# Performance work log

Measured on AMD Instinct MI355X. Metric: run time of the kernel, lower is better.

## Reference

```python
import jax, jax.numpy as jnp
import numpy as np
import math

B, N, DIM = 8, 8192, 256
DIM_ATTN, HEAD, RANK = 256, 4, 64
HEAD_DIM = DIM_ATTN // HEAD


def setup_inputs() -> dict:
    key = jax.random.key(0)
    ks = jax.random.split(key, 8)
    x = jax.random.normal(ks[0], (B, N, DIM), dtype=jnp.float32)
    z = jax.random.normal(ks[1], (B, N, DIM), dtype=jnp.float32)
    # nn.Linear(dim, dim_attn): weight (out,in) -> use (in,out) for x @ W
    Wq = jax.random.normal(ks[2], (DIM, DIM_ATTN), dtype=jnp.float32) / np.sqrt(DIM)
    bq = jnp.zeros((DIM_ATTN,), dtype=jnp.float32)
    K = jax.random.normal(ks[3], (RANK, HEAD, HEAD_DIM), dtype=jnp.float32)
    Wv = jax.random.normal(ks[4], (DIM, DIM), dtype=jnp.float32) / np.sqrt(DIM)
    bv = jnp.zeros((DIM,), dtype=jnp.float32)
    alpha = jnp.full((HEAD, 1), math.log(9.0), dtype=jnp.float32)
    beta = jnp.full((HEAD, 1), math.log(0.01), dtype=jnp.float32)
    return {"x": x, "z": z, "Wq": Wq, "bq": bq, "K": K, "Wv": Wv, "bv": bv,
            "alpha": alpha, "beta": beta}


def reference(x, z, Wq, bq, K, Wv, bv, alpha, beta):
    b, n, f = x.shape
    # q: (b, n, head, head_dim)
    q = (z @ Wq + bq).reshape(b, n, HEAD, HEAD_DIM)
    # attn scores over latent rank: (b, n, h, r)
    attn = jnp.einsum('bnhd,rhd->bnhr', q, K) / np.sqrt(HEAD_DIM).astype(np.float32)
    # value projection: (b, n, h, d)
    xv = (x @ Wv + bv).reshape(b, n, HEAD, HEAD_DIM)
    # pool over n with softmax over r: (b, r, h, d)
    pooled = jnp.einsum('bnhr,bnhd->brhd', jax.nn.softmax(attn, axis=-1), xv)
    # redistribute with softmax over n: (b, n, h, d)
    v = jnp.einsum('bnhr,brhd->bnhd', jax.nn.softmax(attn, axis=1), pooled)
    # sigmoid-gated combine; alpha/beta are (head, 1) broadcasting over (h, d)
    out = jax.nn.sigmoid(alpha) * xv + jax.nn.sigmoid(beta) * v
    return out.reshape(b, n, f)
```

## Files before the change

### kernel.cpp

```cpp
#include <hip/hip_runtime.h>
#include <hip/hip_bf16.h>

typedef __hip_bfloat16 bf16;
typedef __attribute__((ext_vector_type(8))) __bf16 bf16x8;
typedef __attribute__((ext_vector_type(4))) float f32x4;

#define BB 8
#define NN 8192
#define DIM 256
#define HEAD 4
#define HD 64
#define RANK 64
#define BN (BB*NN)

__device__ __forceinline__ float b2f(bf16 v){ return __bfloat162float(v); }
__device__ __forceinline__ bf16 f2b(float v){ return __float2bfloat16(v); }
__device__ __forceinline__ unsigned short f2bu(float f){
    bf16 h = __float2bfloat16(f);
    return *(unsigned short*)&h;
}
__device__ __forceinline__ float u2f(unsigned short u){
    unsigned int x = ((unsigned int)u) << 16; return __uint_as_float(x);
}
__device__ __forceinline__ __bf16 f2bb(float f){
    bf16 h = __float2bfloat16(f);
    return *reinterpret_cast<__bf16*>(&h);
}
__device__ __forceinline__ int swz(int k, int outer){
    return (((k >> 3) ^ (outer & 7)) << 3) | (k & 7);
}

__global__ void __launch_bounds__(256) kW(
    const float* __restrict__ Wq, const float* __restrict__ bq,
    const float* __restrict__ Km, const float* __restrict__ Wv,
    unsigned short* __restrict__ WattnT, unsigned short* __restrict__ WvT,
    float* __restrict__ battn, float* __restrict__ pooledZ)
{
    const int c = blockIdx.x;
    const int h = c >> 6, r = c & 63;
    const int t = threadIdx.x;

    {
        int idx = (blockIdx.x*256 + t)*2;
        *(float2*)&pooledZ[idx] = (float2){0.f, 0.f};
    }

    __shared__ float Ks[64];
    if(t < 64) Ks[t] = Km[((size_t)r*HEAD + h)*64 + t];
    __syncthreads();

    const float* wqrow = Wq + (size_t)t*DIM + h*64;
    float a = 0.f;
    #pragma unroll
    for(int d = 0; d < 64; d++) a = fmaf(wqrow[d], Ks[d], a);
    WattnT[(size_t)c*DIM + t] = f2bu(0.125f * a);
    WvT[(size_t)c*DIM + t]    = f2bu(Wv[(size_t)t*DIM + c]);
    if(t == 0){
        float bb = 0.f;
        for(int d = 0; d < 64; d++) bb += bq[h*64+d]*Ks[d];
        battn[c] = 0.125f * bb;
    }
}

__global__ void __launch_bounds__(256) kG(
    const float* __restrict__ x, const float* __restrict__ z,
    const unsigned short* __restrict__ WvT, const unsigned short* __restrict__ WattnT,
    const float* __restrict__ bv, const float* __restrict__ battn,
    float* __restrict__ outF, unsigned short* __restrict__ outB,
    float* __restrict__ Pm, float* __restrict__ Ps)
{
    __shared__ __attribute__((aligned(16))) __bf16 As8[8][64][40];

    const int role = blockIdx.x & 1;
    const int tile = blockIdx.x >> 1;

    const float* A            = role ? z : x;
    const unsigned short* WT  = role ? WattnT : WvT;
    const float* bias         = role ? battn : bv;

    const int t    = threadIdx.x;
    const int lane = t & 63;
    const int w    = t >> 6;
    const int q    = lane >> 4;
    const int l15  = lane & 15;
    const int brow = tile * 64;
    const int arow = t >> 2, aseg = t & 3;

    const float* aSrc = A + (size_t)(brow + arow)*DIM + aseg*8;
    const unsigned short* bBase = WT + (size_t)(w*64 + l15)*DIM + q*8;

    bf16x8 b0[4], b1[4];
    #pragma unroll
    for(int tn = 0; tn < 4; tn++)
        b0[tn] = *(const bf16x8*)(bBase + (size_t)tn*16*DIM);
    #pragma unroll
    for(int tn = 0; tn < 4; tn++)
        b1[tn] = *(const bf16x8*)(bBase + (size_t)tn*16*DIM + 32);

    #pragma unroll
    for(int s = 0; s < 8; s++){
        float4 v0 = *(const float4*)(aSrc + s*32);
        float4 v1 = *(const float4*)(aSrc + s*32 + 4);
        __attribute__((aligned(16))) __bf16 tmp[8] = {
            f2bb(v0.x), f2bb(v0.y), f2bb(v0.z), f2bb(v0.w),
            f2bb(v1.x), f2bb(v1.y), f2bb(v1.z), f2bb(v1.w)};
        *(bf16x8*)&As8[s][arow][aseg*8] = *(bf16x8*)tmp;
    }

    f32x4 acc[4][4];
    #pragma unroll
    for(int tm = 0; tm < 4; tm++)
        #pragma unroll
        for(int tn = 0; tn < 4; tn++) acc[tm][tn] = (f32x4){0.f,0.f,0.f,0.f};

    __syncthreads();

    #pragma unroll
    for(int step = 0; step < 8; step++){
        bf16x8 b2[4];
        if(step < 6){
            #pragma unroll
            for(int tn = 0; tn < 4; tn++)
                b2[tn] = *(const bf16x8*)(bBase + (size_t)tn*16*DIM + (step+2)*32);
        }

        bf16x8 af[4];
        #pragma unroll
        for(int tm = 0; tm < 4; tm++)
            af[tm] = *(const bf16x8*)&As8[step][tm*16 + l15][q*8];

        #pragma unroll
        for(int tm = 0; tm < 4; tm++)
            #pragma unroll
            for(int tn = 0; tn < 4; tn++)
                acc[tm][tn] = __builtin_amdgcn_mfma_f32_16x16x32_bf16(
                    af[tm], b0[tn], acc[tm][tn], 0, 0, 0);

        #pragma unroll
        for(int tn = 0; tn < 4; tn++){ b0[tn] = b1[tn]; b1[tn] = b2[tn]; }
    }

    if(role){
        const int b  = brow >> 13;
        const int nb = brow & 8191;
        const size_t blk = tile;
        #pragma unroll
        for(int tn = 0; tn < 4; tn++){
            int col = w*64 + tn*16 + l15;
            int hh = col >> 6, rr = col & 63;
            float bcol = bias[col];
            float rv[16];
            float m16 = -1e30f;
            #pragma unroll
            for(int tm = 0; tm < 4; tm++){
                #pragma unroll
                for(int reg = 0; reg < 4; reg++){
                    float v = acc[tm][tn][reg] + bcol;
                    unsigned short ub = f2bu(v);
                    int n = nb + tm*16 + q*4 + reg;
                    outB[(((size_t)(b*HEAD + hh))*NN + n)*64 + rr] = ub;
                    float vr = u2f(ub);
                    rv[tm*4+reg] = vr;
                    m16 = fmaxf(m16, vr);
                }
            }
            float s16 = 0.f;
            #pragma unroll
            for(int i = 0; i < 16; i++) s16 += __expf(rv[i] - m16);
            #pragma unroll
            for(int off = 16; off <= 32; off <<= 1){
                float m2 = __shfl_xor(m16, off, 64);
                float s2 = __shfl_xor(s16, off, 64);
                float nm = fmaxf(m16, m2);
                s16 = s16*__expf(m16-nm) + s2*__expf(m2-nm);
                m16 = nm;
            }
            if(q == 0){
                Pm[blk*256 + col] = m16;
                Ps[blk*256 + col] = s16;
            }
        }
    } else {
        #pragma unroll
        for(int tn = 0; tn < 4; tn++){
            int col = w*64 + tn*16 + l15;
            float bcol = bias[col];
            #pragma unroll
            for(int tm = 0; tm < 4; tm++){
                #pragma unroll
                for(int reg = 0; reg < 4; reg++){
                    int grow = brow + tm*16 + q*4 + reg;
                    outF[(size_t)grow*256 + col] = acc[tm][tn][reg] + bcol;
                }
            }
        }
    }
}

__global__ void __launch_bounds__(256) kD(const unsigned short* __restrict__ attn,
                                          const float* __restrict__ xv,
                                          float* __restrict__ pooledT,
                                          const float* __restrict__ Pm, const float* __restrict__ Ps,
                                          float* __restrict__ Mst, float* __restrict__ Sst)
{
    __shared__ unsigned short s1T[64*256];
    __shared__ unsigned short xvT[64*256];

    const int t = threadIdx.x, lane = t & 63, w = t >> 6;
    const int bh = blockIdx.x, chunk = blockIdx.y;
    const int b = bh >> 2, h = bh & 3;
    const int n0 = chunk * 256;
    const int row = t;

    if(chunk == 0 && (bh & 3) == 0){
        const int bb = bh >> 2, col = t;
        float m = -1e30f;
        for(int c = 0; c < 128; c++)
            m = fmaxf(m, Pm[(size_t)(bb*128 + c)*256 + col]);
        float s = 0.f;
        for(int c = 0; c < 128; c++){
            size_t i = (size_t)(bb*128 + c)*256 + col;
            s += Ps[i] * __expf(Pm[i] - m);
        }
        Mst[bb*256 + col] = m;
        Sst[bb*256 + col] = s;
    }

    {
        const uint4* ap = (const uint4*)(attn + ((size_t)bh*NN + n0 + row)*64);
        uint4 ar[8];
        #pragma unroll
        for(int c = 0; c < 8; c++) ar[c] = ap[c];
        float vals[64];
        #pragma unroll
        for(int c = 0; c < 8; c++){
            unsigned int uu[4] = {ar[c].x, ar[c].y, ar[c].z, ar[c].w};
            #pragma unroll
            for(int p = 0; p < 4; p++){
                vals[c*8 + p*2 + 0] = __uint_as_float(uu[p] << 16);
                vals[c*8 + p*2 + 1] = __uint_as_float(uu[p] & 0xffff0000u);
            }
        }
        float mx = -1e30f;
        #pragma unroll
        for(int r = 0; r < 64; r++) mx = fmaxf(mx, vals[r]);
        float s = 0.f;
        #pragma unroll
        for(int r = 0; r < 64; r++){
            float e = __expf(vals[r] - mx);
            s += e;
            s1T[r*256 + swz(row, r)] = f2bu(e);
        }
        float rs = 1.f / s;
        const float4* xp = (const float4*)(xv + ((size_t)(b*NN + n0 + row))*256 + h*64);
        #pragma unroll
        for(int c = 0; c < 16; c++){
            float4 f = xp[c];
            int d0 = c*4;
            xvT[(d0+0)*256 + swz(row, d0+0)] = f2bu(f.x * rs);
            xvT[(d0+1)*256 + swz(row, d0+1)] = f2bu(f.y * rs);
            xvT[(d0+2)*256 + swz(row, d0+2)] = f2bu(f.z * rs);
            xvT[(d0+3)*256 + swz(row, d0+3)] = f2bu(f.w * rs);
        }
    }
    __syncthreads();

    const int q = lane >> 4, l15 = lane & 15;
    const int dm = w*16 + l15;
    f32x4 acc[4];
    #pragma unroll
    for(int tn = 0; tn < 4; tn++) acc[tn] = (f32x4){0.f,0.f,0.f,0.f};

    #pragma unroll
    for(int slab = 0; slab < 8; slab++){
        int c = slab*4 + q;
        bf16x8 a = *(const bf16x8*)&xvT[dm*256 + ((c ^ (dm & 7))<<3)];
        #pragma unroll
        for(int tn = 0; tn < 4; tn++){
            int rn = tn*16 + l15;
            bf16x8 bb = *(const bf16x8*)&s1T[rn*256 + ((c ^ (rn & 7))<<3)];
            acc[tn] = __builtin_amdgcn_mfma_f32_16x16x32_bf16(a, bb, acc[tn], 0, 0, 0);
        }
    }
    #pragma unroll
    for(int tn = 0; tn < 4; tn++){
        #pragma unroll
        for(int reg = 0; reg < 4; reg++){
            int d = w*16 + q*4 + reg;
            int r = tn*16 + l15;
            atomicAdd(&pooledT[((size_t)bh*64 + d)*64 + r], acc[tn][reg]);
        }
    }
}

__global__ void __launch_bounds__(256) kE(const unsigned short* __restrict__ attn,
                                          const float* __restrict__ xvin,
                                          const float* __restrict__ pooledT,
                                          const float* __restrict__ Mst, const float* __restrict__ Sst,
                                          const float* __restrict__ alpha, const float* __restrict__ beta,
                                          float* __restrict__ out)
{
    __shared__ unsigned short s2t[256*64];
    __shared__ unsigned short plT[64*64];
    __shared__ float Ms[64], Sinv[64];

    const int t = threadIdx.x, lane = t & 63, w = t >> 6;
    const int bh = blockIdx.x, chunk = blockIdx.y;
    const int b = bh >> 2, h = bh & 3;
    const int n0 = chunk * 256;
    const int row = t;

    if(t < 64){
        Ms[t]   = Mst[b*256 + h*64 + t];
        Sinv[t] = 1.f / Sst[b*256 + h*64 + t];
    }
    {
        int d = t >> 2, seg = t & 3;
        const float4* pp = (const float4*)(pooledT + ((size_t)bh*64 + d)*64 + seg*16);
        float4 p0 = pp[0], p1 = pp[1], p2 = pp[2], p3 = pp[3];
        __attribute__((aligned(16))) unsigned short tmp[16] = {
            f2bu(p0.x),f2bu(p0.y),f2bu(p0.z),f2bu(p0.w),
            f2bu(p1.x),f2bu(p1.y),f2bu(p1.z),f2bu(p1.w),
            f2bu(p2.x),f2bu(p2.y),f2bu(p2.z),f2bu(p2.w),
            f2bu(p3.x),f2bu(p3.y),f2bu(p3.z),f2bu(p3.w)};
        int c0 = seg*2;
        *(uint4*)&plT[d*64 + (((c0+0) ^ (d&7))<<3)] = *(uint4*)&tmp[0];
        *(uint4*)&plT[d*64 + (((c0+1) ^ (d&7))<<3)] = *(uint4*)&tmp[8];
    }
    __syncthreads();

    {
        const uint4* ap = (const uint4*)(attn + ((size_t)bh*NN + n0 + row)*64);
        #pragma unroll
        for(int c = 0; c < 8; c++){
            uint4 u = ap[c];
            unsigned int uu[4] = {u.x, u.y, u.z, u.w};
            unsigned int ov[4];
            #pragma unroll
            for(int p = 0; p < 4; p++){
                int r = c*8 + p*2;
                float v0 = __uint_as_float(uu[p] << 16);
                float v1 = __uint_as_float(uu[p] & 0xffff0000u);
                float e0 = __expf(v0 - Ms[r])   * Sinv[r];
                float e1 = __expf(v1 - Ms[r+1]) * Sinv[r+1];
                ov[p] = (unsigned int)f2bu(e0) | ((unsigned int)f2bu(e1) << 16);
            }
            uint4 w4; w4.x = ov[0]; w4.y = ov[1]; w4.z = ov[2]; w4.w = ov[3];
            *(uint4*)&s2t[row*64 + ((c ^ (row&7))<<3)] = w4;
        }
    }
    __syncthreads();

    const int q = lane >> 4, l15 = lane & 15;
    f32x4 acc[4][4];
    #pragma unroll
    for(int tm = 0; tm < 4; tm++)
        #pragma unroll
        for(int tn = 0; tn < 4; tn++) acc[tm][tn] = (f32x4){0.f,0.f,0.f,0.f};

    #pragma unroll
    for(int s = 0; s < 2; s++){
        int c = s*4 + q;
        bf16x8 bfr[4], af[4];
        #pragma unroll
        for(int tn = 0; tn < 4; tn++){
            int dn = tn*16 + l15;
            bfr[tn] = *(const bf16x8*)&plT[dn*64 + ((c ^ (dn&7))<<3)];
        }
        #pragma unroll
        for(int tm = 0; tm < 4; tm++){
            int ra = w*64 + tm*16 + l15;
            af[tm] = *(const bf16x8*)&s2t[ra*64 + ((c ^ (ra&7))<<3)];
        }
        #pragma unroll
        for(int tm = 0; tm < 4; tm++)
            #pragma unroll
            for(int tn = 0; tn < 4; tn++)
                acc[tm][tn] = __builtin_amdgcn_mfma_f32_16x16x32_bf16(
                    af[tm], bfr[tn], acc[tm][tn], 0, 0, 0);
    }

    const float sa = 1.f / (1.f + __expf(-alpha[h]));
    const float sb = 1.f / (1.f + __expf(-beta[h]));
    #pragma unroll
    for(int tm = 0; tm < 4; tm++){
        #pragma unroll
        for(int reg = 0; reg < 4; reg++){
            int rowo = w*64 + tm*16 + q*4 + reg;
            size_t gbase = ((size_t)(b*NN + n0 + rowo))*256 + h*64;
            #pragma unroll
            for(int tn = 0; tn < 4; tn++){
                int d = tn*16 + l15;
                out[gbase + d] = sa*xvin[gbase + d] + sb*acc[tm][tn][reg];
            }
        }
    }
}

extern "C" void kernel_launch(void* const* d_in, const int* in_sizes, int n_in,
                              void* d_out, int out_size, void* d_ws, size_t ws_size,
                              hipStream_t stream)
{
    (void)in_sizes; (void)n_in; (void)out_size; (void)ws_size;
    const float* x     = (const float*)d_in[0];
    const float* z     = (const float*)d_in[1];
    const float* Wq    = (const float*)d_in[2];
    const float* bq    = (const float*)d_in[3];
    const float* Km    = (const float*)d_in[4];
    const float* Wv    = (const float*)d_in[5];
    const float* bv    = (const float*)d_in[6];
    const float* alpha = (const float*)d_in[7];
    const float* beta  = (const float*)d_in[8];
    float* out = (float*)d_out;

    float* xv = out;

    char* ws = (char*)d_ws;
    unsigned short* attn  = (unsigned short*)(ws + 0);
    float* pooledT = (float*)(ws + 33554432);
    float* Mst     = (float*)(ws + 34078720);
    float* Sst     = (float*)(ws + 34086912);
    float* Pm      = (float*)(ws + 34095104);
    float* Ps      = (float*)(ws + 35143680);
    unsigned short* WattnT = (unsigned short*)(ws + 36192256);
    unsigned short* WvT    = (unsigned short*)(ws + 36323328);
    float* battn   = (float*)(ws + 36454400);

    kW<<<dim3(256), 256, 0, stream>>>(Wq, bq, Km, Wv, WattnT, WvT, battn, pooledT);
    kG<<<dim3(2*BN/64), 256, 0, stream>>>(x, z, WvT, WattnT, bv, battn, xv, attn, Pm, Ps);
    kD<<<dim3(32, 32), 256, 0, stream>>>(attn, xv, pooledT, Pm, Ps, Mst, Sst);
    kE<<<dim3(32, 32), 256, 0, stream>>>(attn, xv, pooledT, Mst, Sst, alpha, beta, out);
}
```

Measured before the change: 289.3 us.

## Process two row chunks per block in kD/kE with register prefetch of attn

kD and kE now handle two consecutive 256-row chunks per workgroup, halving the grid's y dimension. The attn rows for the second chunk are loaded into registers before the barrier, overlapping their global latency with the first chunk's MFMA work and output. In kD the xv loads are issued earlier into registers. This trades fewer, longer blocks and extra register pressure for hidden load latency and less per-block setup (e.g. the pooled tile conversion in kE).

New measurement: 310.7 us. 7.4% more time.

```diff
diff --git a/kernel.cpp b/kernel.cpp
--- a/kernel.cpp
+++ b/kernel.cpp
@@ -207,12 +207,12 @@
     __shared__ unsigned short xvT[64*256];
 
     const int t = threadIdx.x, lane = t & 63, w = t >> 6;
-    const int bh = blockIdx.x, chunk = blockIdx.y;
+    const int bh = blockIdx.x, cpair = blockIdx.y;
     const int b = bh >> 2, h = bh & 3;
-    const int n0 = chunk * 256;
     const int row = t;
-
-    if(chunk == 0 && (bh & 3) == 0){
+    const int q = lane >> 4, l15 = lane & 15;
+
+    if(cpair == 0 && (bh & 3) == 0){
         const int bb = bh >> 2, col = t;
         float m = -1e30f;
         for(int c = 0; c < 128; c++)
@@ -226,70 +226,91 @@
         Sst[bb*256 + col] = s;
     }
 
+    uint4 arA[8];
     {
-        const uint4* ap = (const uint4*)(attn + ((size_t)bh*NN + n0 + row)*64);
-        uint4 ar[8];
-        #pragma unroll
-        for(int c = 0; c < 8; c++) ar[c] = ap[c];
-        float vals[64];
+        const uint4* ap = (const uint4*)(attn + ((size_t)bh*NN + cpair*512 + row)*64);
+        #pragma unroll
+        for(int c = 0; c < 8; c++) arA[c] = ap[c];
+    }
+
+    #pragma unroll 1
+    for(int ci = 0; ci < 2; ci++){
+        const int n0 = cpair*512 + ci*256;
+
+        float mx = -1e30f;
         #pragma unroll
         for(int c = 0; c < 8; c++){
-            unsigned int uu[4] = {ar[c].x, ar[c].y, ar[c].z, ar[c].w};
+            unsigned int uu[4] = {arA[c].x, arA[c].y, arA[c].z, arA[c].w};
             #pragma unroll
             for(int p = 0; p < 4; p++){
-                vals[c*8 + p*2 + 0] = __uint_as_float(uu[p] << 16);
-                vals[c*8 + p*2 + 1] = __uint_as_float(uu[p] & 0xffff0000u);
-            }
-        }
-        float mx = -1e30f;
-        #pragma unroll
-        for(int r = 0; r < 64; r++) mx = fmaxf(mx, vals[r]);
+                mx = fmaxf(mx, __uint_as_float(uu[p] << 16));
+                mx = fmaxf(mx, __uint_as_float(uu[p] & 0xffff0000u));
+            }
+        }
+        float4 xf[16];
+        {
+            const float4* xp = (const float4*)(xv + ((size_t)(b*NN + n0 + row))*256 + h*64);
+            #pragma unroll
+            for(int c = 0; c < 16; c++) xf[c] = xp[c];
+        }
         float s = 0.f;
         #pragma unroll
-        for(int r = 0; r < 64; r++){
-            float e = __expf(vals[r] - mx);
-            s += e;
-            s1T[r*256 + swz(row, r)] = f2bu(e);
+        for(int c = 0; c < 8; c++){
+            unsigned int uu[4] = {arA[c].x, arA[c].y, arA[c].z, arA[c].w};
+            #pragma unroll
+            for(int p = 0; p < 4; p++){
+                int r0 = c*8 + p*2;
+                float e0 = __expf(__uint_as_float(uu[p] << 16)        - mx);
+                float e1 = __expf(__uint_as_float(uu[p] & 0xffff0000u) - mx);
+                s += e0 + e1;
+                s1T[(r0+0)*256 + swz(row, r0+0)] = f2bu(e0);
+                s1T[(r0+1)*256 + swz(row, r0+1)] = f2bu(e1);
+            }
         }
         float rs = 1.f / s;
-        const float4* xp = (const float4*)(xv + ((size_t)(b*NN + n0 + row))*256 + h*64);
         #pragma unroll
         for(int c = 0; c < 16; c++){
-            float4 f = xp[c];
+            float4 f = xf[c];
             int d0 = c*4;
             xvT[(d0+0)*256 + swz(row, d0+0)] = f2bu(f.x * rs);
             xvT[(d0+1)*256 + swz(row, d0+1)] = f2bu(f.y * rs);
             xvT[(d0+2)*256 + swz(row, d0+2)] = f2bu(f.z * rs);
             xvT[(d0+3)*256 + swz(row, d0+3)] = f2bu(f.w * rs);
         }
-    }
-    __syncthreads();
-
-    const int q = lane >> 4, l15 = lane & 15;
-    const int dm = w*16 + l15;
-    f32x4 acc[4];
-    #pragma unroll
-    for(int tn = 0; tn < 4; tn++) acc[tn] = (f32x4){0.f,0.f,0.f,0.f};
-
-    #pragma unroll
-    for(int slab = 0; slab < 8; slab++){
-        int c = slab*4 + q;
-        bf16x8 a = *(const bf16x8*)&xvT[dm*256 + ((c ^ (dm & 7))<<3)];
+
+        if(ci == 0){
+            const uint4* ap = (const uint4*)(attn + ((size_t)bh*NN + n0 + 256 + row)*64);
+            #pragma unroll
+            for(int c = 0; c < 8; c++) arA[c] = ap[c];
+        }
+        __syncthreads();
+
+        const int dm = w*16 + l15;
+        f32x4 acc[4];
+        #pragma unroll
+        for(int tn = 0; tn < 4; tn++) acc[tn] = (f32x4){0.f,0.f,0.f,0.f};
+
+        #pragma unroll
+        for(int slab = 0; slab < 8; slab++){
+            int c = slab*4 + q;
+            bf16x8 a = *(const bf16x8*)&xvT[dm*256 + ((c ^ (dm & 7))<<3)];
+            #pragma unroll
+            for(int tn = 0; tn < 4; tn++){
+                int rn = tn*16 + l15;
+                bf16x8 bb2 = *(const bf16x8*)&s1T[rn*256 + ((c ^ (rn & 7))<<3)];
+                acc[tn] = __builtin_amdgcn_mfma_f32_16x16x32_bf16(a, bb2, acc[tn], 0, 0, 0);
+            }
+        }
         #pragma unroll
         for(int tn = 0; tn < 4; tn++){
-            int rn = tn*16 + l15;
-            bf16x8 bb = *(const bf16x8*)&s1T[rn*256 + ((c ^ (rn & 7))<<3)];
-            acc[tn] = __builtin_amdgcn_mfma_f32_16x16x32_bf16(a, bb, acc[tn], 0, 0, 0);
-        }
-    }
-    #pragma unroll
-    for(int tn = 0; tn < 4; tn++){
-        #pragma unroll
-        for(int reg = 0; reg < 4; reg++){
-            int d = w*16 + q*4 + reg;
-            int r = tn*16 + l15;
-            atomicAdd(&pooledT[((size_t)bh*64 + d)*64 + r], acc[tn][reg]);
-        }
+            #pragma unroll
+            for(int reg = 0; reg < 4; reg++){
+                int d = w*16 + q*4 + reg;
+                int r = tn*16 + l15;
+                atomicAdd(&pooledT[((size_t)bh*64 + d)*64 + r], acc[tn][reg]);
+            }
+        }
+        if(ci == 0) __syncthreads();
     }
 }
 
@@ -305,10 +326,10 @@
     __shared__ float Ms[64], Sinv[64];
 
     const int t = threadIdx.x, lane = t & 63, w = t >> 6;
-    const int bh = blockIdx.x, chunk = blockIdx.y;
+    const int bh = blockIdx.x, cpair = blockIdx.y;
     const int b = bh >> 2, h = bh & 3;
-    const int n0 = chunk * 256;
     const int row = t;
+    const int q = lane >> 4, l15 = lane & 15;
 
     if(t < 64){
         Ms[t]   = Mst[b*256 + h*64 + t];
@@ -327,13 +348,25 @@
         *(uint4*)&plT[d*64 + (((c0+0) ^ (d&7))<<3)] = *(uint4*)&tmp[0];
         *(uint4*)&plT[d*64 + (((c0+1) ^ (d&7))<<3)] = *(uint4*)&tmp[8];
     }
+
+    uint4 arA[8];
+    {
+        const uint4* ap = (const uint4*)(attn + ((size_t)bh*NN + cpair*512 + row)*64);
+        #pragma unroll
+        for(int c = 0; c < 8; c++) arA[c] = ap[c];
+    }
     __syncthreads();
 
-    {
-        const uint4* ap = (const uint4*)(attn + ((size_t)bh*NN + n0 + row)*64);
+    const float sa = 1.f / (1.f + __expf(-alpha[h]));
+    const float sb = 1.f / (1.f + __expf(-beta[h]));
+
+    #pragma unroll 1
+    for(int ci = 0; ci < 2; ci++){
+        const int n0 = cpair*512 + ci*256;
+
         #pragma unroll
         for(int c = 0; c < 8; c++){
-            uint4 u = ap[c];
+            uint4 u = arA[c];
             unsigned int uu[4] = {u.x, u.y, u.z, u.w};
             unsigned int ov[4];
             #pragma unroll
@@ -348,52 +381,56 @@
             uint4 w4; w4.x = ov[0]; w4.y = ov[1]; w4.z = ov[2]; w4.w = ov[3];
             *(uint4*)&s2t[row*64 + ((c ^ (row&7))<<3)] = w4;
         }
-    }
-    __syncthreads();
-
-    const int q = lane >> 4, l15 = lane & 15;
-    f32x4 acc[4][4];
-    #pragma unroll
-    for(int tm = 0; tm < 4; tm++)
-        #pragma unroll
-        for(int tn = 0; tn < 4; tn++) acc[tm][tn] = (f32x4){0.f,0.f,0.f,0.f};
-
-    #pragma unroll
-    for(int s = 0; s < 2; s++){
-        int c = s*4 + q;
-        bf16x8 bfr[4], af[4];
-        #pragma unroll
-        for(int tn = 0; tn < 4; tn++){
-            int dn = tn*16 + l15;
-            bfr[tn] = *(const bf16x8*)&plT[dn*64 + ((c ^ (dn&7))<<3)];
-        }
+
+        if(ci == 0){
+            const uint4* ap = (const uint4*)(attn + ((size_t)bh*NN + n0 + 256 + row)*64);
+            #pragma unroll
+            for(int c = 0; c < 8; c++) arA[c] = ap[c];
+        }
+        __syncthreads();
+
+        f32x4 acc[4][4];
+        #pragma unroll
+        for(int tm = 0; tm < 4; tm++)
+            #pragma unroll
+            for(int tn = 0; tn < 4; tn++) acc[tm][tn] = (f32x4){0.f,0.f,0.f,0.f};
+
+        #pragma unroll
+        for(int s = 0; s < 2; s++){
+            int c = s*4 + q;
+            bf16x8 bfr[4], af[4];
+            #pragma unroll
+            for(int tn = 0; tn < 4; tn++){
+                int dn = tn*16 + l15;
+                bfr[tn] = *(const bf16x8*)&plT[dn*64 + ((c ^ (dn&7))<<3)];
+            }
+            #pragma unroll
+            for(int tm = 0; tm < 4; tm++){
+                int ra = w*64 + tm*16 + l15;
+                af[tm] = *(const bf16x8*)&s2t[ra*64 + ((c ^ (ra&7))<<3)];
+            }
+            #pragma unroll
+            for(int tm = 0; tm < 4; tm++)
+                #pragma unroll
+                for(int tn = 0; tn < 4; tn++)
+                    acc[tm][tn] = __builtin_amdgcn_mfma_f32_16x16x32_bf16(
+                        af[tm], bfr[tn], acc[tm][tn], 0, 0, 0);
+        }
+
         #pragma unroll
         for(int tm = 0; tm < 4; tm++){
-            int ra = w*64 + tm*16 + l15;
-            af[tm] = *(const bf16x8*)&s2t[ra*64 + ((c ^ (ra&7))<<3)];
-        }
-        #pragma unroll
-        for(int tm = 0; tm < 4; tm++)
-            #pragma unroll
-            for(int tn = 0; tn < 4; tn++)
-                acc[tm][tn] = __builtin_amdgcn_mfma_f32_16x16x32_bf16(
-                    af[tm], bfr[tn], acc[tm][tn], 0, 0, 0);
-    }
-
-    const float sa = 1.f / (1.f + __expf(-alpha[h]));
-    const float sb = 1.f / (1.f + __expf(-beta[h]));
-    #pragma unroll
-    for(int tm = 0; tm < 4; tm++){
-        #pragma unroll
-        for(int reg = 0; reg < 4; reg++){
-            int rowo = w*64 + tm*16 + q*4 + reg;
-            size_t gbase = ((size_t)(b*NN + n0 + rowo))*256 + h*64;
-            #pragma unroll
-            for(int tn = 0; tn < 4; tn++){
-                int d = tn*16 + l15;
-                out[gbase + d] = sa*xvin[gbase + d] + sb*acc[tm][tn][reg];
-            }
-        }
+            #pragma unroll
+            for(int reg = 0; reg < 4; reg++){
+                int rowo = w*64 + tm*16 + q*4 + reg;
+                size_t gbase = ((size_t)(b*NN + n0 + rowo))*256 + h*64;
+                #pragma unroll
+                for(int tn = 0; tn < 4; tn++){
+                    int d = tn*16 + l15;
+                    out[gbase + d] = sa*xvin[gbase + d] + sb*acc[tm][tn][reg];
+                }
+            }
+        }
+        if(ci == 0) __syncthreads();
     }
 }
 
@@ -428,6 +465,6 @@
 
     kW<<<dim3(256), 256, 0, stream>>>(Wq, bq, Km, Wv, WattnT, WvT, battn, pooledT);
     kG<<<dim3(2*BN/64), 256, 0, stream>>>(x, z, WvT, WattnT, bv, battn, xv, attn, Pm, Ps);
-    kD<<<dim3(32, 32), 256, 0, stream>>>(attn, xv, pooledT, Pm, Ps, Mst, Sst);
-    kE<<<dim3(32, 32), 256, 0, stream>>>(attn, xv, pooledT, Mst, Sst, alpha, beta, out);
-}
+    kD<<<dim3(32, 16), 256, 0, stream>>>(attn, xv, pooledT, Pm, Ps, Mst, Sst);
+    kE<<<dim3(32, 16), 256, 0, stream>>>(attn, xv, pooledT, Mst, Sst, alpha, beta, out);
+}
```
